# Optimization experiments

Hardware: AMD Instinct MI355X
Metric: run time of the kernel (lower is better)

## Reference

```python
import jax, jax.numpy as jnp
import numpy as np

N_CELLS = 2048
D_IN = 512
D_HID = 1024
D_OUT = 512
SYNC = 0.15
DEBATE = 0.15
N_FACTIONS = 8


def setup_inputs() -> dict:
    key = jax.random.key(0)
    ks = jax.random.split(key, 24)
    def w(k, shape, s=0.02):
        return jax.random.normal(k, shape, dtype=jnp.float32) * s
    ein = D_IN + D_HID          # complex-engine input dim (1536)
    gin = D_OUT + 1 + D_HID     # GRU gate input dim (1537)
    return {
        "x": jax.random.normal(ks[0], (1, D_IN), dtype=jnp.float32),
        "h_re": w(ks[1], (N_CELLS, D_HID), 0.1),
        "h_im": w(ks[2], (N_CELLS, D_HID), 0.1),
        "ea_wr": w(ks[3], (ein, D_OUT)), "ea_br": w(ks[4], (D_OUT,)),
        "ea_wi": w(ks[5], (ein, D_OUT)), "ea_bi": w(ks[6], (D_OUT,)),
        "eg_wr": w(ks[7], (ein, D_OUT)), "eg_br": w(ks[8], (D_OUT,)),
        "eg_wi": w(ks[9], (ein, D_OUT)), "eg_bi": w(ks[10], (D_OUT,)),
        "gz_w": w(ks[11], (gin, D_HID)), "gz_b": w(ks[12], (D_HID,)),
        "gr_w": w(ks[13], (gin, D_HID)), "gr_b": w(ks[14], (D_HID,)),
        "ghr_w": w(ks[15], (gin, D_HID)), "ghr_b": w(ks[16], (D_HID,)),
        "ghi_w": w(ks[17], (gin, D_HID)), "ghi_b": w(ks[18], (D_HID,)),
        "oh_w": w(ks[19], (2 * D_OUT, D_IN)), "oh_b": w(ks[20], (D_IN,)),
        "step": 7,
    }


def _clin(a, b, Wr, br, Wi, bi):
    # complex linear: (Wr + iWi)(a + ib) with torch's bias semantics
    return (a @ Wr + br) - (b @ Wi + bi), (b @ Wr + br) + (a @ Wi + bi)


def reference(x, h_re, h_im, ea_wr, ea_br, ea_wi, ea_bi, eg_wr, eg_br, eg_wi, eg_bi,
              gz_w, gz_b, gr_w, gr_b, ghr_w, ghr_b, ghi_w, ghi_b, oh_w, oh_b, step):
    # batch the 256-cell Python loop into single GEMMs over the cell axis
    xb = jnp.broadcast_to(x, (N_CELLS, D_IN))
    c_re = jnp.concatenate([xb, h_re], -1)                       # [N, D_IN+D_HID]
    c_im = jnp.concatenate([jnp.zeros_like(xb), h_im], -1)
    a_re, a_im = _clin(c_re, c_im, ea_wr, ea_br, ea_wi, ea_bi)
    g_re, g_im = _clin(c_re, c_im, eg_wr, eg_br, eg_wi, eg_bi)
    o_re, o_im = a_re - g_re, a_im - g_im                        # [N, D_OUT]
    tension = jnp.mean(o_re**2 + o_im**2, -1)                    # [N]

    # GRU memory update (detached input, matching output.detach())
    so_re = jax.lax.stop_gradient(o_re)
    so_im = jax.lax.stop_gradient(o_im)
    t_sg = jax.lax.stop_gradient(tension)
    mem_re = jnp.concatenate([so_re, t_sg[:, None]], -1)         # [N, D_OUT+1]
    mem_im = jnp.concatenate([so_im, jnp.zeros((N_CELLS, 1), o_im.dtype)], -1)
    x_mag = jnp.sqrt(mem_re**2 + mem_im**2)
    h_mag = jnp.sqrt(h_re**2 + h_im**2)
    cm = jnp.concatenate([x_mag, h_mag], -1)                     # [N, D_OUT+1+D_HID]
    z = jax.nn.sigmoid(cm @ gz_w + gz_b)
    r = jax.nn.sigmoid(cm @ gr_w + gr_b)
    comb_r = jnp.concatenate([mem_re, r * h_re], -1)
    comb_i = jnp.concatenate([mem_im, r * h_im], -1)
    cand_re = jnp.tanh(comb_r @ ghr_w + ghr_b)
    cand_im = jnp.tanh(comb_i @ ghi_w + ghi_b)
    nh_re = jax.lax.stop_gradient((1 - z) * h_re + z * cand_re)
    nh_im = jax.lax.stop_gradient((1 - z) * h_im + z * cand_im)

    # faction sync + debate (linear op, applied per component)
    fs = N_CELLS // N_FACTIONS
    def sync(h):
        hf = h.reshape(N_FACTIONS, fs, D_HID)
        hf = (1 - SYNC) * hf + SYNC * jnp.mean(hf, 1, keepdims=True)
        if step > 5:
            glob = jnp.mean(jnp.mean(hf, 1), 0)                  # [D_HID]
            dc = max(1, fs // 4)
            hf = hf.at[:, :dc].set((1 - DEBATE) * hf[:, :dc] + DEBATE * glob)
        return hf.reshape(N_CELLS, D_HID)
    nh_re, nh_im = sync(nh_re), sync(nh_im)

    # tension-softmax-weighted combination (weights are non-differentiable, .item() in torch)
    w_soft = jax.nn.softmax(t_sg)                                # [N]
    comb_re = (w_soft[:, None] * o_re).sum(0, keepdims=True)     # [1, D_OUT]
    comb_im = (w_soft[:, None] * o_im).sum(0, keepdims=True)
    out_real = jnp.concatenate([comb_re, comb_im], -1)           # [1, 2*D_OUT]
    pred = out_real @ oh_w + oh_b                                # [1, D_IN]
    return pred, jnp.mean(tension), nh_re, nh_im
```

## Files before the change

kernel.cpp:

```cpp
#include <hip/hip_runtime.h>
#include <math.h>

#define N_CELLS 2048
#define D_IN 512
#define D_HID 1024
#define D_OUT 512

typedef __attribute__((ext_vector_type(8))) short bf16x8;
typedef __attribute__((ext_vector_type(4))) float f32x4;
typedef __attribute__((ext_vector_type(4))) short short4v;

#define MFMA16(a, b, c) __builtin_amdgcn_mfma_f32_16x16x32_bf16(a, b, c, 0, 0, 0)

__device__ __forceinline__ short f2bf(float f) {
  union { float f; unsigned u; } v; v.f = f;
  unsigned r = (v.u + 0x7FFFu + ((v.u >> 16) & 1u)) >> 16;
  return (short)r;
}

__device__ __forceinline__ float bf2f(unsigned short u) {
  union { unsigned u; float f; } v; v.u = ((unsigned)u) << 16; return v.f;
}

__device__ __forceinline__ void gl_lds16(const void* g, void* l) {
  __builtin_amdgcn_global_load_lds(
      (const __attribute__((address_space(1))) void*)g,
      (__attribute__((address_space(3))) void*)l, 16, 0, 0);
}

__global__ __launch_bounds__(256) void k_prep_all(
    const float* __restrict__ w0, const float* __restrict__ w1,
    const float* __restrict__ w2, const float* __restrict__ w3,
    short* __restrict__ t0, short* __restrict__ t1,
    short* __restrict__ t2, short* __restrict__ t3,
    const float* __restrict__ ea_wr, const float* __restrict__ eg_wr,
    const float* __restrict__ ea_wi, const float* __restrict__ eg_wi,
    short* __restrict__ wdrT, short* __restrict__ wdiT, short* __restrict__ wdnT,
    const float* __restrict__ h_re, const float* __restrict__ h_im,
    short* __restrict__ hbre, short* __restrict__ hbim, short* __restrict__ gatesA,
    float* __restrict__ tens,
    const float* __restrict__ x,
    float* __restrict__ bpartr, float* __restrict__ bparti,
    float* __restrict__ fsbuf) {
  __shared__ float ts0[32][33], ts1[32][33];
  const int bx = blockIdx.x;
  const int tid = threadIdx.x;
  if (bx < 6144) {
    const int z = bx / 1536, idx = bx % 1536;
    const int xx = idx % 48, yy = idx / 48;
    const float* w = (z == 0) ? w0 : (z == 1) ? w1 : (z == 2) ? w2 : w3;
    short* wT = (z == 0) ? t0 : (z == 1) ? t1 : (z == 2) ? t2 : t3;
    const int k0 = xx * 32, n0 = yy * 32;
    const int c = tid & 31, r4 = tid >> 5;
#pragma unroll
    for (int i = 0; i < 4; ++i) {
      int kl = r4 * 4 + i;
      int k = k0 + kl;
      int srcrow = (k < 512) ? k : k + 1;
      ts0[kl][c] = w[(size_t)srcrow * D_HID + n0 + c];
    }
    __syncthreads();
#pragma unroll
    for (int i = 0; i < 4; ++i) {
      int nl = r4 * 4 + i;
      wT[(size_t)(n0 + nl) * 1536 + k0 + c] = f2bf(ts0[c][nl]);
    }
  } else if (bx < 6656) {
    const int idx = bx - 6144;
    const int xx = idx & 31, yy = idx >> 5;
    const int k0 = xx * 32, n0 = yy * 32;
    const int c = tid & 31, r4 = tid >> 5;
#pragma unroll
    for (int i = 0; i < 4; ++i) {
      int kl = r4 * 4 + i;
      int src = (512 + k0 + kl) * D_OUT + n0 + c;
      ts0[kl][c] = ea_wr[src] - eg_wr[src];
      ts1[kl][c] = ea_wi[src] - eg_wi[src];
    }
    __syncthreads();
#pragma unroll
    for (int i = 0; i < 4; ++i) {
      int nl = r4 * 4 + i;
      int dst = (n0 + nl) * D_HID + k0 + c;
      float dr = ts0[c][nl], di = ts1[c][nl];
      wdrT[dst] = f2bf(dr);
      wdiT[dst] = f2bf(di);
      wdnT[dst] = f2bf(-di);
    }
  } else if (bx < 8704) {
    const int idx = bx - 6656;
    if (tid == 0) tens[idx] = 0.f;
    int idx4 = (idx * 256 + tid) * 4;
    int m = idx4 >> 10, n = idx4 & 1023;
    float4 hr = *(const float4*)&h_re[idx4];
    float4 hi = *(const float4*)&h_im[idx4];
    short4v br, bi, bm;
    br.x = f2bf(hr.x); br.y = f2bf(hr.y); br.z = f2bf(hr.z); br.w = f2bf(hr.w);
    bi.x = f2bf(hi.x); bi.y = f2bf(hi.y); bi.z = f2bf(hi.z); bi.w = f2bf(hi.w);
    bm.x = f2bf(sqrtf(hr.x * hr.x + hi.x * hi.x));
    bm.y = f2bf(sqrtf(hr.y * hr.y + hi.y * hi.y));
    bm.z = f2bf(sqrtf(hr.z * hr.z + hi.z * hi.z));
    bm.w = f2bf(sqrtf(hr.w * hr.w + hi.w * hi.w));
    *(short4v*)&hbre[idx4] = br;
    *(short4v*)&hbim[idx4] = bi;
    *(short4v*)&gatesA[(size_t)m * 1536 + 512 + n] = bm;
  } else if (bx < 8720) {
    const int idx = bx - 8704;
    int n = (idx & 1) * 256 + tid;
    int kc = idx >> 1;
    float sr = 0.f, si = 0.f;
    for (int i = 0; i < 64; ++i) {
      int k = kc * 64 + i;
      float xv = x[k];
      int j = k * D_OUT + n;
      sr += xv * (ea_wr[j] - eg_wr[j]);
      si += xv * (ea_wi[j] - eg_wi[j]);
    }
    bpartr[kc * D_OUT + n] = sr;
    bparti[kc * D_OUT + n] = si;
  } else {
    const int idx = bx - 8720;
    int i = idx * 1024 + tid * 4;
    *(float4*)&fsbuf[i] = (float4){0.f, 0.f, 0.f, 0.f};
  }
}

__global__ __launch_bounds__(256) void k_engine(
    const short* __restrict__ hbre, const short* __restrict__ hbim,
    const short* __restrict__ wdrT, const short* __restrict__ wdiT,
    const short* __restrict__ wdnT,
    const float* __restrict__ bpartr, const float* __restrict__ bparti,
    const float* __restrict__ ea_br, const float* __restrict__ ea_bi,
    const float* __restrict__ eg_br, const float* __restrict__ eg_bi,
    float* __restrict__ ore, float* __restrict__ oim,
    short* __restrict__ gatesA, short* __restrict__ candAre, short* __restrict__ candAim,
    float* __restrict__ tens) {
  __shared__ short Ar[2 * 64 * 32], Ai[2 * 64 * 32];
  __shared__ short Brs[2 * 32 * 32], Bis[2 * 32 * 32], Bns[2 * 32 * 32];
  const int m0 = blockIdx.x * 64, n0 = blockIdx.y * 32;
  const int tid = threadIdx.x;
  const int wid = tid >> 6, lane = tid & 63;
  const int quad = lane >> 4, lcol = lane & 15;
  const int wm = wid * 16;
  f32x4 accre[2], accim[2];
#pragma unroll
  for (int nt = 0; nt < 2; ++nt) {
    accre[nt] = (f32x4){0.f, 0.f, 0.f, 0.f};
    accim[nt] = (f32x4){0.f, 0.f, 0.f, 0.f};
  }
  for (int k0 = 0; k0 < D_HID; k0 += 64) {
    if (k0) __syncthreads();
#pragma unroll
    for (int i = 0; i < 2; ++i) {
      int c = i * 256 + tid;
      int kh = c >> 8, row = (c >> 2) & 63, kq = c & 3;
      size_t g = (size_t)(m0 + row) * D_HID + k0 + kh * 32 + kq * 8;
      gl_lds16(hbre + g, &Ar[c * 8]);
      gl_lds16(hbim + g, &Ai[c * 8]);
    }
    {
      int c = tid;
      int kh = c >> 7, row = (c >> 2) & 31, kq = c & 3;
      size_t g = (size_t)(n0 + row) * D_HID + k0 + kh * 32 + kq * 8;
      gl_lds16(wdrT + g, &Brs[c * 8]);
      gl_lds16(wdiT + g, &Bis[c * 8]);
      gl_lds16(wdnT + g, &Bns[c * 8]);
    }
    __syncthreads();
#pragma unroll
    for (int kh = 0; kh < 2; ++kh) {
      bf16x8 ar, ai, br[2], bi[2], bn[2];
      int aoff = kh * 2048 + (wm + lcol) * 32 + quad * 8;
      ar = *(const bf16x8*)&Ar[aoff];
      ai = *(const bf16x8*)&Ai[aoff];
#pragma unroll
      for (int nt = 0; nt < 2; ++nt) {
        int boff = kh * 1024 + (nt * 16 + lcol) * 32 + quad * 8;
        br[nt] = *(const bf16x8*)&Brs[boff];
        bi[nt] = *(const bf16x8*)&Bis[boff];
        bn[nt] = *(const bf16x8*)&Bns[boff];
      }
#pragma unroll
      for (int nt = 0; nt < 2; ++nt) {
        accre[nt] = MFMA16(ar, br[nt], accre[nt]);
        accre[nt] = MFMA16(ai, bn[nt], accre[nt]);
        accim[nt] = MFMA16(ar, bi[nt], accim[nt]);
        accim[nt] = MFMA16(ai, br[nt], accim[nt]);
      }
    }
  }
  float biasre[2], biasim[2];
#pragma unroll
  for (int nt = 0; nt < 2; ++nt) {
    int n = n0 + nt * 16 + lcol;
    float sr = 0.f, si = 0.f;
#pragma unroll
    for (int kc = 0; kc < 8; ++kc) { sr += bpartr[kc * D_OUT + n]; si += bparti[kc * D_OUT + n]; }
    float brd = ea_br[n] - eg_br[n];
    float bid = ea_bi[n] - eg_bi[n];
    biasre[nt] = sr + brd - bid;
    biasim[nt] = si + brd + bid;
  }
#pragma unroll
  for (int r = 0; r < 4; ++r) {
    int m = m0 + wm + quad * 4 + r;
    float t = 0.f;
#pragma unroll
    for (int nt = 0; nt < 2; ++nt) {
      int n = n0 + nt * 16 + lcol;
      float cre = accre[nt][r] + biasre[nt];
      float cim = accim[nt][r] + biasim[nt];
      t += cre * cre + cim * cim;
      ore[(size_t)m * D_OUT + n] = cre;
      oim[(size_t)m * D_OUT + n] = cim;
      gatesA[(size_t)m * 1536 + n] = f2bf(sqrtf(cre * cre + cim * cim));
      candAre[(size_t)m * 1536 + n] = f2bf(cre);
      candAim[(size_t)m * 1536 + n] = f2bf(cim);
    }
#pragma unroll
    for (int off = 1; off < 16; off <<= 1) t += __shfl_xor(t, off);
    if (lcol == 0) atomicAdd(&tens[m], t * (1.f / 512.f));
  }
}

__global__ __launch_bounds__(256) void k_gates(
    const short* __restrict__ gatesA,
    const short* __restrict__ gzwT, const short* __restrict__ grwT,
    const float* __restrict__ gz_w, const float* __restrict__ gz_b,
    const float* __restrict__ gr_w, const float* __restrict__ gr_b,
    const float* __restrict__ tens,
    const float* __restrict__ h_re, const float* __restrict__ h_im,
    unsigned short* __restrict__ zbuf,
    short* __restrict__ candAre, short* __restrict__ candAim) {
  __shared__ short As[2 * 64 * 32];
  __shared__ short Bs[2 * 64 * 32];
  const int is_z = (blockIdx.z == 0);
  const short* Bt = is_z ? gzwT : grwT;
  const int m0 = blockIdx.x * 64, n0 = blockIdx.y * 64;
  const int tid = threadIdx.x;
  const int wid = tid >> 6, lane = tid & 63;
  const int quad = lane >> 4, lcol = lane & 15;
  const int wm = (wid >> 1) * 32, wn = (wid & 1) * 32;
  f32x4 acc[2][2];
#pragma unroll
  for (int mt = 0; mt < 2; ++mt)
#pragma unroll
    for (int nt = 0; nt < 2; ++nt) acc[mt][nt] = (f32x4){0.f, 0.f, 0.f, 0.f};
  for (int k0 = 0; k0 < 1536; k0 += 64) {
    if (k0) __syncthreads();
#pragma unroll
    for (int i = 0; i < 2; ++i) {
      int c = i * 256 + tid;
      int kh = c >> 8, row = (c >> 2) & 63, kq = c & 3;
      gl_lds16(gatesA + (size_t)(m0 + row) * 1536 + k0 + kh * 32 + kq * 8, &As[c * 8]);
      gl_lds16(Bt + (size_t)(n0 + row) * 1536 + k0 + kh * 32 + kq * 8, &Bs[c * 8]);
    }
    __syncthreads();
#pragma unroll
    for (int kh = 0; kh < 2; ++kh) {
      bf16x8 a[2], b[2];
#pragma unroll
      for (int mt = 0; mt < 2; ++mt)
        a[mt] = *(const bf16x8*)&As[kh * 2048 + (wm + mt * 16 + lcol) * 32 + quad * 8];
#pragma unroll
      for (int nt = 0; nt < 2; ++nt)
        b[nt] = *(const bf16x8*)&Bs[kh * 2048 + (wn + nt * 16 + lcol) * 32 + quad * 8];
#pragma unroll
      for (int mt = 0; mt < 2; ++mt)
#pragma unroll
        for (int nt = 0; nt < 2; ++nt)
          acc[mt][nt] = MFMA16(a[mt], b[nt], acc[mt][nt]);
    }
  }
#pragma unroll
  for (int mt = 0; mt < 2; ++mt)
#pragma unroll
    for (int nt = 0; nt < 2; ++nt)
#pragma unroll
      for (int r = 0; r < 4; ++r) {
        int m = m0 + wm + mt * 16 + quad * 4 + r;
        int n = n0 + wn + nt * 16 + lcol;
        float tv = tens[m];
        if (is_z) {
          float zp = acc[mt][nt][r] + gz_b[n] + tv * gz_w[(size_t)512 * D_HID + n];
          zbuf[(size_t)m * D_HID + n] = (unsigned short)f2bf(1.f / (1.f + expf(-zp)));
        } else {
          float rp = acc[mt][nt][r] + gr_b[n] + tv * gr_w[(size_t)512 * D_HID + n];
          float rr = 1.f / (1.f + expf(-rp));
          candAre[(size_t)m * 1536 + 512 + n] = f2bf(rr * h_re[(size_t)m * D_HID + n]);
          candAim[(size_t)m * 1536 + 512 + n] = f2bf(rr * h_im[(size_t)m * D_HID + n]);
        }
      }
}

__global__ __launch_bounds__(256) void k_cand(
    const short* __restrict__ candAre, const short* __restrict__ candAim,
    const short* __restrict__ ghrwT, const short* __restrict__ ghiwT,
    const float* __restrict__ ghr_b, const float* __restrict__ ghi_b,
    const float* __restrict__ ghr_w,
    const float* __restrict__ tens, const unsigned short* __restrict__ zbuf,
    const float* __restrict__ h_re, const float* __restrict__ h_im,
    float* __restrict__ nhre, float* __restrict__ nhim) {
  __shared__ short As[2 * 64 * 32];
  __shared__ short Bs[2 * 64 * 32];
  const int is_re = (blockIdx.z == 0);
  const short* A = is_re ? candAre : candAim;
  const short* Bt = is_re ? ghrwT : ghiwT;
  const float* bias = is_re ? ghr_b : ghi_b;
  const float* h = is_re ? h_re : h_im;
  float* outp = is_re ? nhre : nhim;
  const int m0 = blockIdx.x * 64, n0 = blockIdx.y * 64;
  const int tid = threadIdx.x;
  const int wid = tid >> 6, lane = tid & 63;
  const int quad = lane >> 4, lcol = lane & 15;
  const int wm = (wid >> 1) * 32, wn = (wid & 1) * 32;
  f32x4 acc[2][2];
#pragma unroll
  for (int mt = 0; mt < 2; ++mt)
#pragma unroll
    for (int nt = 0; nt < 2; ++nt) acc[mt][nt] = (f32x4){0.f, 0.f, 0.f, 0.f};
  for (int k0 = 0; k0 < 1536; k0 += 64) {
    if (k0) __syncthreads();
#pragma unroll
    for (int i = 0; i < 2; ++i) {
      int c = i * 256 + tid;
      int kh = c >> 8, row = (c >> 2) & 63, kq = c & 3;
      gl_lds16(A + (size_t)(m0 + row) * 1536 + k0 + kh * 32 + kq * 8, &As[c * 8]);
      gl_lds16(Bt + (size_t)(n0 + row) * 1536 + k0 + kh * 32 + kq * 8, &Bs[c * 8]);
    }
    __syncthreads();
#pragma unroll
    for (int kh = 0; kh < 2; ++kh) {
      bf16x8 a[2], b[2];
#pragma unroll
      for (int mt = 0; mt < 2; ++mt)
        a[mt] = *(const bf16x8*)&As[kh * 2048 + (wm + mt * 16 + lcol) * 32 + quad * 8];
#pragma unroll
      for (int nt = 0; nt < 2; ++nt)
        b[nt] = *(const bf16x8*)&Bs[kh * 2048 + (wn + nt * 16 + lcol) * 32 + quad * 8];
#pragma unroll
      for (int mt = 0; mt < 2; ++mt)
#pragma unroll
        for (int nt = 0; nt < 2; ++nt)
          acc[mt][nt] = MFMA16(a[mt], b[nt], acc[mt][nt]);
    }
  }
#pragma unroll
  for (int mt = 0; mt < 2; ++mt)
#pragma unroll
    for (int nt = 0; nt < 2; ++nt)
#pragma unroll
      for (int r = 0; r < 4; ++r) {
        int m = m0 + wm + mt * 16 + quad * 4 + r;
        int n = n0 + wn + nt * 16 + lcol;
        float pre = acc[mt][nt][r] + bias[n];
        if (is_re) pre += tens[m] * ghr_w[(size_t)512 * D_HID + n];
        float cand = tanhf(pre);
        float z = bf2f(zbuf[(size_t)m * D_HID + n]);
        float hv = h[(size_t)m * D_HID + n];
        outp[(size_t)m * D_HID + n] = (1.f - z) * hv + z * cand;
      }
}

__global__ __launch_bounds__(256) void k_fsum_part(
    const float* __restrict__ nhre, const float* __restrict__ nhim,
    float* __restrict__ fsbuf) {
  int f = blockIdx.x >> 3, rc = blockIdx.x & 7, comp = blockIdx.y;
  const float* src = comp ? nhim : nhre;
  float* fs = fsbuf + (size_t)comp * 8192;
  int row0 = f * 256 + rc * 32;
#pragma unroll
  for (int nc = 0; nc < 4; ++nc) {
    int n = nc * 256 + threadIdx.x;
    float s = 0.f;
    const float* base = src + (size_t)row0 * D_HID + n;
    for (int j = 0; j < 32; ++j) s += base[(size_t)j * D_HID];
    atomicAdd(&fs[(size_t)n * 8 + f], s);
  }
}

__global__ __launch_bounds__(256) void k_sync(
    float* __restrict__ nhre, float* __restrict__ nhim,
    const float* __restrict__ fsbuf, const int* __restrict__ step) {
  int idx = blockIdx.x * 256 + threadIdx.x;
  int m = idx >> 10, n = idx & 1023;
  int f = m >> 8;
  const float* f0 = fsbuf + (size_t)n * 8;
  const float* f1 = fsbuf + 8192 + (size_t)n * 8;
  float gr = 0.f, gi = 0.f;
#pragma unroll
  for (int ff = 0; ff < 8; ++ff) { gr += f0[ff]; gi += f1[ff]; }
  float fr = f0[f], fi = f1[f];
  float vr = nhre[idx], vi = nhim[idx];
  vr = 0.85f * vr + 0.15f * (fr * (1.f / 256.f));
  vi = 0.85f * vi + 0.15f * (fi * (1.f / 256.f));
  if (step[0] > 5 && (m & 255) < 64) {
    vr = 0.85f * vr + 0.15f * (gr * (1.f / 2048.f));
    vi = 0.85f * vi + 0.15f * (gi * (1.f / 2048.f));
  }
  nhre[idx] = vr;
  nhim[idx] = vi;
}

__global__ __launch_bounds__(1024) void k_stats(
    const float* __restrict__ tens, float* __restrict__ wsoft,
    float* __restrict__ meanT_out) {
  __shared__ float red[16];
  __shared__ float s_max, s_sum;
  int tid = threadIdx.x;
  int wid = tid >> 6, lane = tid & 63;
  float a = tens[tid], b = tens[tid + 1024];
  float mx = fmaxf(a, b);
  for (int off = 32; off; off >>= 1) mx = fmaxf(mx, __shfl_down(mx, off));
  if (lane == 0) red[wid] = mx;
  __syncthreads();
  if (tid == 0) {
    float m2 = red[0];
    for (int i = 1; i < 16; ++i) m2 = fmaxf(m2, red[i]);
    s_max = m2;
  }
  __syncthreads();
  float mxv = s_max;
  float ea = expf(a - mxv), eb = expf(b - mxv);
  float se = ea + eb;
  for (int off = 32; off; off >>= 1) se += __shfl_down(se, off);
  __syncthreads();
  if (lane == 0) red[wid] = se;
  __syncthreads();
  if (tid == 0) {
    float s2 = 0.f;
    for (int i = 0; i < 16; ++i) s2 += red[i];
    s_sum = s2;
  }
  __syncthreads();
  float inv = 1.f / s_sum;
  wsoft[tid] = ea * inv;
  wsoft[tid + 1024] = eb * inv;
  float st = a + b;
  for (int off = 32; off; off >>= 1) st += __shfl_down(st, off);
  __syncthreads();
  if (lane == 0) red[wid] = st;
  __syncthreads();
  if (tid == 0) {
    float s2 = 0.f;
    for (int i = 0; i < 16; ++i) s2 += red[i];
    meanT_out[0] = s2 * (1.f / 2048.f);
  }
}

__global__ __launch_bounds__(256) void k_comb_part(
    const float* __restrict__ ore, const float* __restrict__ oim,
    const float* __restrict__ wsoft, float* __restrict__ cpart) {
  int j = blockIdx.x * 256 + threadIdx.x;
  int mc = blockIdx.y;
  const float* src = (j < 512) ? ore : oim;
  int col = j & 511;
  float s = 0.f;
  for (int i = 0; i < 128; ++i) {
    int m = mc * 128 + i;
    s += wsoft[m] * src[(size_t)m * D_OUT + col];
  }
  cpart[(size_t)mc * 1024 + j] = s;
}

__global__ __launch_bounds__(256) void k_pred_part(
    const float* __restrict__ cpart, const float* __restrict__ oh_w,
    float* __restrict__ ppart) {
  __shared__ float combs[128];
  int tid = threadIdx.x;
  int jc = blockIdx.y;
  if (tid < 128) {
    float s = 0.f;
#pragma unroll
    for (int mc = 0; mc < 16; ++mc) s += cpart[(size_t)mc * 1024 + jc * 128 + tid];
    combs[tid] = s;
  }
  __syncthreads();
  int n = blockIdx.x * 256 + tid;
  float s = 0.f;
  for (int i = 0; i < 128; ++i)
    s += combs[i] * oh_w[(size_t)(jc * 128 + i) * D_IN + n];
  ppart[(size_t)jc * D_IN + n] = s;
}

__global__ __launch_bounds__(256) void k_pred_red(
    const float* __restrict__ ppart, const float* __restrict__ oh_b,
    float* __restrict__ pred) {
  int n = blockIdx.x * 256 + threadIdx.x;
  float s = oh_b[n];
#pragma unroll
  for (int jc = 0; jc < 8; ++jc) s += ppart[(size_t)jc * D_IN + n];
  pred[n] = s;
}

extern "C" void kernel_launch(void* const* d_in, const int* in_sizes, int n_in,
                              void* d_out, int out_size, void* d_ws, size_t ws_size,
                              hipStream_t stream) {
  const float* x     = (const float*)d_in[0];
  const float* h_re  = (const float*)d_in[1];
  const float* h_im  = (const float*)d_in[2];
  const float* ea_wr = (const float*)d_in[3];
  const float* ea_br = (const float*)d_in[4];
  const float* ea_wi = (const float*)d_in[5];
  const float* ea_bi = (const float*)d_in[6];
  const float* eg_wr = (const float*)d_in[7];
  const float* eg_br = (const float*)d_in[8];
  const float* eg_wi = (const float*)d_in[9];
  const float* eg_bi = (const float*)d_in[10];
  const float* gz_w  = (const float*)d_in[11];
  const float* gz_b  = (const float*)d_in[12];
  const float* gr_w  = (const float*)d_in[13];
  const float* gr_b  = (const float*)d_in[14];
  const float* ghr_w = (const float*)d_in[15];
  const float* ghr_b = (const float*)d_in[16];
  const float* ghi_w = (const float*)d_in[17];
  const float* ghi_b = (const float*)d_in[18];
  const float* oh_w  = (const float*)d_in[19];
  const float* oh_b  = (const float*)d_in[20];
  const int*   step  = (const int*)d_in[21];

  float* out = (float*)d_out;
  float* pred_out  = out;
  float* meanT_out = out + 512;
  float* nhre_out  = out + 513;
  float* nhim_out  = out + 513 + N_CELLS * D_HID;

  char* p = (char*)d_ws;
  auto carve = [&](size_t bytes) { char* r = p; p += (bytes + 255) & ~(size_t)255; return r; };
  short* wdrT   = (short*)carve(512 * 1024 * 2);
  short* wdiT   = (short*)carve(512 * 1024 * 2);
  short* wdnT   = (short*)carve(512 * 1024 * 2);
  short* gzwT   = (short*)carve(1024 * 1536 * 2);
  short* grwT   = (short*)carve(1024 * 1536 * 2);
  short* ghrwT  = (short*)carve(1024 * 1536 * 2);
  short* ghiwT  = (short*)carve(1024 * 1536 * 2);
  short* hbre   = (short*)carve(2048 * 1024 * 2);
  short* hbim   = (short*)carve(2048 * 1024 * 2);
  short* gatesA = (short*)carve((size_t)2048 * 1536 * 2);
  short* candAre= (short*)carve((size_t)2048 * 1536 * 2);
  short* candAim= (short*)carve((size_t)2048 * 1536 * 2);
  float* ore    = (float*)carve(2048 * 512 * 4);
  float* oim    = (float*)carve(2048 * 512 * 4);
  unsigned short* zbuf = (unsigned short*)carve((size_t)2048 * 1024 * 2);
  float* bpartr = (float*)carve(8 * 512 * 4);
  float* bparti = (float*)carve(8 * 512 * 4);
  float* tens   = (float*)carve(2048 * 4);
  float* fsbuf  = (float*)carve(2 * 8192 * 4);
  float* wsoft  = (float*)carve(2048 * 4);
  float* cpart  = (float*)carve(16 * 1024 * 4);
  float* ppart  = (float*)carve(8 * 512 * 4);

  hipLaunchKernelGGL(k_prep_all, dim3(8736), dim3(256), 0, stream,
                     gz_w, gr_w, ghr_w, ghi_w, gzwT, grwT, ghrwT, ghiwT,
                     ea_wr, eg_wr, ea_wi, eg_wi, wdrT, wdiT, wdnT,
                     h_re, h_im, hbre, hbim, gatesA, tens,
                     x, bpartr, bparti, fsbuf);
  hipLaunchKernelGGL(k_engine, dim3(32, 16), dim3(256), 0, stream,
                     hbre, hbim, wdrT, wdiT, wdnT,
                     bpartr, bparti, ea_br, ea_bi, eg_br, eg_bi,
                     ore, oim, gatesA, candAre, candAim, tens);
  hipLaunchKernelGGL(k_gates, dim3(32, 16, 2), dim3(256), 0, stream,
                     gatesA, gzwT, grwT, gz_w, gz_b, gr_w, gr_b, tens,
                     h_re, h_im, zbuf, candAre, candAim);
  hipLaunchKernelGGL(k_cand, dim3(32, 16, 2), dim3(256), 0, stream,
                     candAre, candAim, ghrwT, ghiwT, ghr_b, ghi_b, ghr_w,
                     tens, zbuf, h_re, h_im, nhre_out, nhim_out);
  hipLaunchKernelGGL(k_fsum_part, dim3(64, 2), dim3(256), 0, stream,
                     nhre_out, nhim_out, fsbuf);
  hipLaunchKernelGGL(k_sync, dim3((N_CELLS * D_HID) / 256), dim3(256), 0, stream,
                     nhre_out, nhim_out, fsbuf, step);
  hipLaunchKernelGGL(k_stats, dim3(1), dim3(1024), 0, stream, tens, wsoft, meanT_out);
  hipLaunchKernelGGL(k_comb_part, dim3(4, 16), dim3(256), 0, stream,
                     ore, oim, wsoft, cpart);
  hipLaunchKernelGGL(k_pred_part, dim3(2, 8), dim3(256), 0, stream, cpart, oh_w, ppart);
  hipLaunchKernelGGL(k_pred_red, dim3(2), dim3(256), 0, stream, ppart, oh_b, pred_out);
}
```

Before: 283.7 us.

## Fuse all stages into one cooperative persistent kernel with grid syncs

Replaces the ten separate launches with a single cooperative kernel of 512 blocks that loops over work units for each stage and separates stages with grid-wide syncs. The original per-stage kernels remain as a fallback. It also drops the precomputed negated-imaginary weight matrix in favour of sign-flipping the A fragment in registers, and merges sync with the comb step. The aim is to remove launch gaps and some memory traffic. In exchange, a 512-block grid on 256 CUs leaves each stage with fewer concurrent blocks than before, and grid syncs carry their own cost.

```diff
diff --git a/kernel.cpp b/kernel.cpp
--- a/kernel.cpp
+++ b/kernel.cpp
@@ -1,5 +1,8 @@
 #include <hip/hip_runtime.h>
+#include <hip/hip_cooperative_groups.h>
 #include <math.h>
+
+namespace cg = cooperative_groups;
 
 #define N_CELLS 2048
 #define D_IN 512
@@ -22,78 +25,89 @@
   union { unsigned u; float f; } v; v.u = ((unsigned)u) << 16; return v.f;
 }
 
+__device__ __forceinline__ bf16x8 neg8(bf16x8 v) {
+  union { bf16x8 s; unsigned u[4]; } a; a.s = v;
+#pragma unroll
+  for (int i = 0; i < 4; ++i) a.u[i] ^= 0x80008000u;
+  return a.s;
+}
+
 __device__ __forceinline__ void gl_lds16(const void* g, void* l) {
   __builtin_amdgcn_global_load_lds(
       (const __attribute__((address_space(1))) void*)g,
       (__attribute__((address_space(3))) void*)l, 16, 0, 0);
 }
 
-__global__ __launch_bounds__(256) void k_prep_all(
-    const float* __restrict__ w0, const float* __restrict__ w1,
-    const float* __restrict__ w2, const float* __restrict__ w3,
-    short* __restrict__ t0, short* __restrict__ t1,
-    short* __restrict__ t2, short* __restrict__ t3,
-    const float* __restrict__ ea_wr, const float* __restrict__ eg_wr,
-    const float* __restrict__ ea_wi, const float* __restrict__ eg_wi,
-    short* __restrict__ wdrT, short* __restrict__ wdiT, short* __restrict__ wdnT,
-    const float* __restrict__ h_re, const float* __restrict__ h_im,
-    short* __restrict__ hbre, short* __restrict__ hbim, short* __restrict__ gatesA,
-    float* __restrict__ tens,
-    const float* __restrict__ x,
-    float* __restrict__ bpartr, float* __restrict__ bparti,
-    float* __restrict__ fsbuf) {
-  __shared__ float ts0[32][33], ts1[32][33];
-  const int bx = blockIdx.x;
-  const int tid = threadIdx.x;
-  if (bx < 6144) {
-    const int z = bx / 1536, idx = bx % 1536;
+struct P {
+  const float *x, *h_re, *h_im;
+  const float *ea_wr, *ea_br, *ea_wi, *ea_bi;
+  const float *eg_wr, *eg_br, *eg_wi, *eg_bi;
+  const float *gz_w, *gz_b, *gr_w, *gr_b;
+  const float *ghr_w, *ghr_b, *ghi_w, *ghi_b;
+  const float *oh_w, *oh_b;
+  const int *step;
+  short *wdrT, *wdiT, *gzwT, *grwT, *ghrwT, *ghiwT;
+  short *hbre, *hbim, *gatesA, *candAre, *candAim;
+  float *ore, *oim;
+  unsigned short *zbuf;
+  float *bpartr, *bparti, *tens, *fsbuf, *wsoft, *cpart, *ppart;
+  float *pred_out, *meanT_out, *nhre, *nhim;
+};
+
+
+__device__ __forceinline__ void dev_prep(const P& p, int u, int tid, short* lds) {
+  if (u < 6144) {
+    float* ts0 = (float*)lds;
+    const int z = u / 1536, idx = u % 1536;
     const int xx = idx % 48, yy = idx / 48;
-    const float* w = (z == 0) ? w0 : (z == 1) ? w1 : (z == 2) ? w2 : w3;
-    short* wT = (z == 0) ? t0 : (z == 1) ? t1 : (z == 2) ? t2 : t3;
+    const float* w = (z == 0) ? p.gz_w : (z == 1) ? p.gr_w : (z == 2) ? p.ghr_w : p.ghi_w;
+    short* wT = (z == 0) ? p.gzwT : (z == 1) ? p.grwT : (z == 2) ? p.ghrwT : p.ghiwT;
     const int k0 = xx * 32, n0 = yy * 32;
     const int c = tid & 31, r4 = tid >> 5;
+    __syncthreads();
 #pragma unroll
     for (int i = 0; i < 4; ++i) {
       int kl = r4 * 4 + i;
       int k = k0 + kl;
       int srcrow = (k < 512) ? k : k + 1;
-      ts0[kl][c] = w[(size_t)srcrow * D_HID + n0 + c];
+      ts0[kl * 33 + c] = w[(size_t)srcrow * D_HID + n0 + c];
     }
     __syncthreads();
 #pragma unroll
     for (int i = 0; i < 4; ++i) {
       int nl = r4 * 4 + i;
-      wT[(size_t)(n0 + nl) * 1536 + k0 + c] = f2bf(ts0[c][nl]);
-    }
-  } else if (bx < 6656) {
-    const int idx = bx - 6144;
+      wT[(size_t)(n0 + nl) * 1536 + k0 + c] = f2bf(ts0[c * 33 + nl]);
+    }
+  } else if (u < 6656) {
+    float* ts0 = (float*)lds;
+    float* ts1 = ts0 + 32 * 33;
+    const int idx = u - 6144;
     const int xx = idx & 31, yy = idx >> 5;
     const int k0 = xx * 32, n0 = yy * 32;
     const int c = tid & 31, r4 = tid >> 5;
+    __syncthreads();
 #pragma unroll
     for (int i = 0; i < 4; ++i) {
       int kl = r4 * 4 + i;
       int src = (512 + k0 + kl) * D_OUT + n0 + c;
-      ts0[kl][c] = ea_wr[src] - eg_wr[src];
-      ts1[kl][c] = ea_wi[src] - eg_wi[src];
+      ts0[kl * 33 + c] = p.ea_wr[src] - p.eg_wr[src];
+      ts1[kl * 33 + c] = p.ea_wi[src] - p.eg_wi[src];
     }
     __syncthreads();
 #pragma unroll
     for (int i = 0; i < 4; ++i) {
       int nl = r4 * 4 + i;
       int dst = (n0 + nl) * D_HID + k0 + c;
-      float dr = ts0[c][nl], di = ts1[c][nl];
-      wdrT[dst] = f2bf(dr);
-      wdiT[dst] = f2bf(di);
-      wdnT[dst] = f2bf(-di);
-    }
-  } else if (bx < 8704) {
-    const int idx = bx - 6656;
-    if (tid == 0) tens[idx] = 0.f;
+      p.wdrT[dst] = f2bf(ts0[c * 33 + nl]);
+      p.wdiT[dst] = f2bf(ts1[c * 33 + nl]);
+    }
+  } else if (u < 8704) {
+    const int idx = u - 6656;
+    if (tid == 0) p.tens[idx] = 0.f;
     int idx4 = (idx * 256 + tid) * 4;
     int m = idx4 >> 10, n = idx4 & 1023;
-    float4 hr = *(const float4*)&h_re[idx4];
-    float4 hi = *(const float4*)&h_im[idx4];
+    float4 hr = *(const float4*)&p.h_re[idx4];
+    float4 hi = *(const float4*)&p.h_im[idx4];
     short4v br, bi, bm;
     br.x = f2bf(hr.x); br.y = f2bf(hr.y); br.z = f2bf(hr.z); br.w = f2bf(hr.w);
     bi.x = f2bf(hi.x); bi.y = f2bf(hi.y); bi.z = f2bf(hi.z); bi.w = f2bf(hi.w);
@@ -101,46 +115,38 @@
     bm.y = f2bf(sqrtf(hr.y * hr.y + hi.y * hi.y));
     bm.z = f2bf(sqrtf(hr.z * hr.z + hi.z * hi.z));
     bm.w = f2bf(sqrtf(hr.w * hr.w + hi.w * hi.w));
-    *(short4v*)&hbre[idx4] = br;
-    *(short4v*)&hbim[idx4] = bi;
-    *(short4v*)&gatesA[(size_t)m * 1536 + 512 + n] = bm;
-  } else if (bx < 8720) {
-    const int idx = bx - 8704;
+    *(short4v*)&p.hbre[idx4] = br;
+    *(short4v*)&p.hbim[idx4] = bi;
+    *(short4v*)&p.gatesA[(size_t)m * 1536 + 512 + n] = bm;
+  } else if (u < 8720) {
+    const int idx = u - 8704;
     int n = (idx & 1) * 256 + tid;
     int kc = idx >> 1;
     float sr = 0.f, si = 0.f;
     for (int i = 0; i < 64; ++i) {
       int k = kc * 64 + i;
-      float xv = x[k];
+      float xv = p.x[k];
       int j = k * D_OUT + n;
-      sr += xv * (ea_wr[j] - eg_wr[j]);
-      si += xv * (ea_wi[j] - eg_wi[j]);
-    }
-    bpartr[kc * D_OUT + n] = sr;
-    bparti[kc * D_OUT + n] = si;
+      sr += xv * (p.ea_wr[j] - p.eg_wr[j]);
+      si += xv * (p.ea_wi[j] - p.eg_wi[j]);
+    }
+    p.bpartr[kc * D_OUT + n] = sr;
+    p.bparti[kc * D_OUT + n] = si;
   } else {
-    const int idx = bx - 8720;
+    const int idx = u - 8720;
     int i = idx * 1024 + tid * 4;
-    *(float4*)&fsbuf[i] = (float4){0.f, 0.f, 0.f, 0.f};
-  }
-}
-
-__global__ __launch_bounds__(256) void k_engine(
-    const short* __restrict__ hbre, const short* __restrict__ hbim,
-    const short* __restrict__ wdrT, const short* __restrict__ wdiT,
-    const short* __restrict__ wdnT,
-    const float* __restrict__ bpartr, const float* __restrict__ bparti,
-    const float* __restrict__ ea_br, const float* __restrict__ ea_bi,
-    const float* __restrict__ eg_br, const float* __restrict__ eg_bi,
-    float* __restrict__ ore, float* __restrict__ oim,
-    short* __restrict__ gatesA, short* __restrict__ candAre, short* __restrict__ candAim,
-    float* __restrict__ tens) {
-  __shared__ short Ar[2 * 64 * 32], Ai[2 * 64 * 32];
-  __shared__ short Brs[2 * 32 * 32], Bis[2 * 32 * 32], Bns[2 * 32 * 32];
-  const int m0 = blockIdx.x * 64, n0 = blockIdx.y * 32;
-  const int tid = threadIdx.x;
+    *(float4*)&p.fsbuf[i] = (float4){0.f, 0.f, 0.f, 0.f};
+  }
+}
+
+__device__ __forceinline__ void dev_engine(const P& p, int unit, int tid, short* lds) {
+  short* Ar = lds;
+  short* Ai = lds + 4096;
+  short* Brs = lds + 8192;
+  short* Bis = lds + 10240;
   const int wid = tid >> 6, lane = tid & 63;
   const int quad = lane >> 4, lcol = lane & 15;
+  const int m0 = (unit & 31) * 64, n0 = (unit >> 5) * 32;
   const int wm = wid * 16;
   f32x4 accre[2], accim[2];
 #pragma unroll
@@ -149,27 +155,26 @@
     accim[nt] = (f32x4){0.f, 0.f, 0.f, 0.f};
   }
   for (int k0 = 0; k0 < D_HID; k0 += 64) {
-    if (k0) __syncthreads();
+    __syncthreads();
 #pragma unroll
     for (int i = 0; i < 2; ++i) {
       int c = i * 256 + tid;
       int kh = c >> 8, row = (c >> 2) & 63, kq = c & 3;
       size_t g = (size_t)(m0 + row) * D_HID + k0 + kh * 32 + kq * 8;
-      gl_lds16(hbre + g, &Ar[c * 8]);
-      gl_lds16(hbim + g, &Ai[c * 8]);
+      gl_lds16(p.hbre + g, &Ar[c * 8]);
+      gl_lds16(p.hbim + g, &Ai[c * 8]);
     }
     {
       int c = tid;
       int kh = c >> 7, row = (c >> 2) & 31, kq = c & 3;
       size_t g = (size_t)(n0 + row) * D_HID + k0 + kh * 32 + kq * 8;
-      gl_lds16(wdrT + g, &Brs[c * 8]);
-      gl_lds16(wdiT + g, &Bis[c * 8]);
-      gl_lds16(wdnT + g, &Bns[c * 8]);
+      gl_lds16(p.wdrT + g, &Brs[c * 8]);
+      gl_lds16(p.wdiT + g, &Bis[c * 8]);
     }
     __syncthreads();
 #pragma unroll
     for (int kh = 0; kh < 2; ++kh) {
-      bf16x8 ar, ai, br[2], bi[2], bn[2];
+      bf16x8 ar, ai, br[2], bi[2];
       int aoff = kh * 2048 + (wm + lcol) * 32 + quad * 8;
       ar = *(const bf16x8*)&Ar[aoff];
       ai = *(const bf16x8*)&Ai[aoff];
@@ -178,12 +183,12 @@
         int boff = kh * 1024 + (nt * 16 + lcol) * 32 + quad * 8;
         br[nt] = *(const bf16x8*)&Brs[boff];
         bi[nt] = *(const bf16x8*)&Bis[boff];
-        bn[nt] = *(const bf16x8*)&Bns[boff];
       }
+      bf16x8 ani = neg8(ai);
 #pragma unroll
       for (int nt = 0; nt < 2; ++nt) {
         accre[nt] = MFMA16(ar, br[nt], accre[nt]);
-        accre[nt] = MFMA16(ai, bn[nt], accre[nt]);
+        accre[nt] = MFMA16(ani, bi[nt], accre[nt]);
         accim[nt] = MFMA16(ar, bi[nt], accim[nt]);
         accim[nt] = MFMA16(ai, br[nt], accim[nt]);
       }
@@ -195,9 +200,9 @@
     int n = n0 + nt * 16 + lcol;
     float sr = 0.f, si = 0.f;
 #pragma unroll
-    for (int kc = 0; kc < 8; ++kc) { sr += bpartr[kc * D_OUT + n]; si += bparti[kc * D_OUT + n]; }
-    float brd = ea_br[n] - eg_br[n];
-    float bid = ea_bi[n] - eg_bi[n];
+    for (int kc = 0; kc < 8; ++kc) { sr += p.bpartr[kc * D_OUT + n]; si += p.bparti[kc * D_OUT + n]; }
+    float brd = p.ea_br[n] - p.eg_br[n];
+    float bid = p.ea_bi[n] - p.eg_bi[n];
     biasre[nt] = sr + brd - bid;
     biasim[nt] = si + brd + bid;
   }
@@ -211,35 +216,27 @@
       float cre = accre[nt][r] + biasre[nt];
       float cim = accim[nt][r] + biasim[nt];
       t += cre * cre + cim * cim;
-      ore[(size_t)m * D_OUT + n] = cre;
-      oim[(size_t)m * D_OUT + n] = cim;
-      gatesA[(size_t)m * 1536 + n] = f2bf(sqrtf(cre * cre + cim * cim));
-      candAre[(size_t)m * 1536 + n] = f2bf(cre);
-      candAim[(size_t)m * 1536 + n] = f2bf(cim);
+      p.ore[(size_t)m * D_OUT + n] = cre;
+      p.oim[(size_t)m * D_OUT + n] = cim;
+      p.gatesA[(size_t)m * 1536 + n] = f2bf(sqrtf(cre * cre + cim * cim));
+      p.candAre[(size_t)m * 1536 + n] = f2bf(cre);
+      p.candAim[(size_t)m * 1536 + n] = f2bf(cim);
     }
 #pragma unroll
     for (int off = 1; off < 16; off <<= 1) t += __shfl_xor(t, off);
-    if (lcol == 0) atomicAdd(&tens[m], t * (1.f / 512.f));
-  }
-}
-
-__global__ __launch_bounds__(256) void k_gates(
-    const short* __restrict__ gatesA,
-    const short* __restrict__ gzwT, const short* __restrict__ grwT,
-    const float* __restrict__ gz_w, const float* __restrict__ gz_b,
-    const float* __restrict__ gr_w, const float* __restrict__ gr_b,
-    const float* __restrict__ tens,
-    const float* __restrict__ h_re, const float* __restrict__ h_im,
-    unsigned short* __restrict__ zbuf,
-    short* __restrict__ candAre, short* __restrict__ candAim) {
-  __shared__ short As[2 * 64 * 32];
-  __shared__ short Bs[2 * 64 * 32];
-  const int is_z = (blockIdx.z == 0);
-  const short* Bt = is_z ? gzwT : grwT;
-  const int m0 = blockIdx.x * 64, n0 = blockIdx.y * 64;
-  const int tid = threadIdx.x;
+    if (lcol == 0) atomicAdd(&p.tens[m], t * (1.f / 512.f));
+  }
+}
+
+__device__ __forceinline__ void dev_gates(const P& p, int unit, int tid, short* lds) {
+  short* As = lds;
+  short* Bs = lds + 4096;
+  const int is_z = (unit < 512);
+  const int bb = unit & 511;
+  const short* Bt = is_z ? p.gzwT : p.grwT;
   const int wid = tid >> 6, lane = tid & 63;
   const int quad = lane >> 4, lcol = lane & 15;
+  const int m0 = (bb & 31) * 64, n0 = (bb >> 5) * 64;
   const int wm = (wid >> 1) * 32, wn = (wid & 1) * 32;
   f32x4 acc[2][2];
 #pragma unroll
@@ -247,12 +244,12 @@
 #pragma unroll
     for (int nt = 0; nt < 2; ++nt) acc[mt][nt] = (f32x4){0.f, 0.f, 0.f, 0.f};
   for (int k0 = 0; k0 < 1536; k0 += 64) {
-    if (k0) __syncthreads();
+    __syncthreads();
 #pragma unroll
     for (int i = 0; i < 2; ++i) {
       int c = i * 256 + tid;
       int kh = c >> 8, row = (c >> 2) & 63, kq = c & 3;
-      gl_lds16(gatesA + (size_t)(m0 + row) * 1536 + k0 + kh * 32 + kq * 8, &As[c * 8]);
+      gl_lds16(p.gatesA + (size_t)(m0 + row) * 1536 + k0 + kh * 32 + kq * 8, &As[c * 8]);
       gl_lds16(Bt + (size_t)(n0 + row) * 1536 + k0 + kh * 32 + kq * 8, &Bs[c * 8]);
     }
     __syncthreads();
@@ -280,39 +277,32 @@
       for (int r = 0; r < 4; ++r) {
         int m = m0 + wm + mt * 16 + quad * 4 + r;
         int n = n0 + wn + nt * 16 + lcol;
-        float tv = tens[m];
+        float tv = p.tens[m];
         if (is_z) {
-          float zp = acc[mt][nt][r] + gz_b[n] + tv * gz_w[(size_t)512 * D_HID + n];
-          zbuf[(size_t)m * D_HID + n] = (unsigned short)f2bf(1.f / (1.f + expf(-zp)));
+          float zp = acc[mt][nt][r] + p.gz_b[n] + tv * p.gz_w[(size_t)512 * D_HID + n];
+          p.zbuf[(size_t)m * D_HID + n] = (unsigned short)f2bf(1.f / (1.f + expf(-zp)));
         } else {
-          float rp = acc[mt][nt][r] + gr_b[n] + tv * gr_w[(size_t)512 * D_HID + n];
+          float rp = acc[mt][nt][r] + p.gr_b[n] + tv * p.gr_w[(size_t)512 * D_HID + n];
           float rr = 1.f / (1.f + expf(-rp));
-          candAre[(size_t)m * 1536 + 512 + n] = f2bf(rr * h_re[(size_t)m * D_HID + n]);
-          candAim[(size_t)m * 1536 + 512 + n] = f2bf(rr * h_im[(size_t)m * D_HID + n]);
+          p.candAre[(size_t)m * 1536 + 512 + n] = f2bf(rr * p.h_re[(size_t)m * D_HID + n]);
+          p.candAim[(size_t)m * 1536 + 512 + n] = f2bf(rr * p.h_im[(size_t)m * D_HID + n]);
         }
       }
 }
 
-__global__ __launch_bounds__(256) void k_cand(
-    const short* __restrict__ candAre, const short* __restrict__ candAim,
-    const short* __restrict__ ghrwT, const short* __restrict__ ghiwT,
-    const float* __restrict__ ghr_b, const float* __restrict__ ghi_b,
-    const float* __restrict__ ghr_w,
-    const float* __restrict__ tens, const unsigned short* __restrict__ zbuf,
-    const float* __restrict__ h_re, const float* __restrict__ h_im,
-    float* __restrict__ nhre, float* __restrict__ nhim) {
-  __shared__ short As[2 * 64 * 32];
-  __shared__ short Bs[2 * 64 * 32];
-  const int is_re = (blockIdx.z == 0);
-  const short* A = is_re ? candAre : candAim;
-  const short* Bt = is_re ? ghrwT : ghiwT;
-  const float* bias = is_re ? ghr_b : ghi_b;
-  const float* h = is_re ? h_re : h_im;
-  float* outp = is_re ? nhre : nhim;
-  const int m0 = blockIdx.x * 64, n0 = blockIdx.y * 64;
-  const int tid = threadIdx.x;
+__device__ __forceinline__ void dev_cand(const P& p, int unit, int tid, short* lds) {
+  short* As = lds;
+  short* Bs = lds + 4096;
+  const int is_re = (unit < 512);
+  const int bb = unit & 511;
+  const short* A = is_re ? p.candAre : p.candAim;
+  const short* Bt = is_re ? p.ghrwT : p.ghiwT;
+  const float* bias = is_re ? p.ghr_b : p.ghi_b;
+  const float* h = is_re ? p.h_re : p.h_im;
+  float* outp = is_re ? p.nhre : p.nhim;
   const int wid = tid >> 6, lane = tid & 63;
   const int quad = lane >> 4, lcol = lane & 15;
+  const int m0 = (bb & 31) * 64, n0 = (bb >> 5) * 64;
   const int wm = (wid >> 1) * 32, wn = (wid & 1) * 32;
   f32x4 acc[2][2];
 #pragma unroll
@@ -320,7 +310,7 @@
 #pragma unroll
     for (int nt = 0; nt < 2; ++nt) acc[mt][nt] = (f32x4){0.f, 0.f, 0.f, 0.f};
   for (int k0 = 0; k0 < 1536; k0 += 64) {
-    if (k0) __syncthreads();
+    __syncthreads();
 #pragma unroll
     for (int i = 0; i < 2; ++i) {
       int c = i * 256 + tid;
@@ -354,24 +344,22 @@
         int m = m0 + wm + mt * 16 + quad * 4 + r;
         int n = n0 + wn + nt * 16 + lcol;
         float pre = acc[mt][nt][r] + bias[n];
-        if (is_re) pre += tens[m] * ghr_w[(size_t)512 * D_HID + n];
+        if (is_re) pre += p.tens[m] * p.ghr_w[(size_t)512 * D_HID + n];
         float cand = tanhf(pre);
-        float z = bf2f(zbuf[(size_t)m * D_HID + n]);
+        float z = bf2f(p.zbuf[(size_t)m * D_HID + n]);
         float hv = h[(size_t)m * D_HID + n];
         outp[(size_t)m * D_HID + n] = (1.f - z) * hv + z * cand;
       }
 }
 
-__global__ __launch_bounds__(256) void k_fsum_part(
-    const float* __restrict__ nhre, const float* __restrict__ nhim,
-    float* __restrict__ fsbuf) {
-  int f = blockIdx.x >> 3, rc = blockIdx.x & 7, comp = blockIdx.y;
-  const float* src = comp ? nhim : nhre;
-  float* fs = fsbuf + (size_t)comp * 8192;
+__device__ __forceinline__ void dev_fsum(const P& p, int unit, int tid) {
+  int f = (unit & 63) >> 3, rc = unit & 7, comp = unit >> 6;
+  const float* src = comp ? p.nhim : p.nhre;
+  float* fs = p.fsbuf + (size_t)comp * 8192;
   int row0 = f * 256 + rc * 32;
 #pragma unroll
   for (int nc = 0; nc < 4; ++nc) {
-    int n = nc * 256 + threadIdx.x;
+    int n = nc * 256 + tid;
     float s = 0.f;
     const float* base = src + (size_t)row0 * D_HID + n;
     for (int j = 0; j < 32; ++j) s += base[(size_t)j * D_HID];
@@ -379,157 +367,159 @@
   }
 }
 
-__global__ __launch_bounds__(256) void k_sync(
-    float* __restrict__ nhre, float* __restrict__ nhim,
-    const float* __restrict__ fsbuf, const int* __restrict__ step) {
-  int idx = blockIdx.x * 256 + threadIdx.x;
-  int m = idx >> 10, n = idx & 1023;
-  int f = m >> 8;
-  const float* f0 = fsbuf + (size_t)n * 8;
-  const float* f1 = fsbuf + 8192 + (size_t)n * 8;
-  float gr = 0.f, gi = 0.f;
-#pragma unroll
-  for (int ff = 0; ff < 8; ++ff) { gr += f0[ff]; gi += f1[ff]; }
-  float fr = f0[f], fi = f1[f];
-  float vr = nhre[idx], vi = nhim[idx];
-  vr = 0.85f * vr + 0.15f * (fr * (1.f / 256.f));
-  vi = 0.85f * vi + 0.15f * (fi * (1.f / 256.f));
-  if (step[0] > 5 && (m & 255) < 64) {
-    vr = 0.85f * vr + 0.15f * (gr * (1.f / 2048.f));
-    vi = 0.85f * vi + 0.15f * (gi * (1.f / 2048.f));
-  }
-  nhre[idx] = vr;
-  nhim[idx] = vi;
-}
-
-__global__ __launch_bounds__(1024) void k_stats(
-    const float* __restrict__ tens, float* __restrict__ wsoft,
-    float* __restrict__ meanT_out) {
-  __shared__ float red[16];
-  __shared__ float s_max, s_sum;
-  int tid = threadIdx.x;
-  int wid = tid >> 6, lane = tid & 63;
-  float a = tens[tid], b = tens[tid + 1024];
-  float mx = fmaxf(a, b);
-  for (int off = 32; off; off >>= 1) mx = fmaxf(mx, __shfl_down(mx, off));
+__device__ __forceinline__ void dev_stats(const P& p, int tid, short* lds) {
+  float* red = (float*)lds;
+  const int wid = tid >> 6, lane = tid & 63;
+  float v[8];
+  float mx = -1e30f;
+#pragma unroll
+  for (int k2 = 0; k2 < 8; ++k2) { v[k2] = p.tens[tid + 256 * k2]; mx = fmaxf(mx, v[k2]); }
+  for (int off = 1; off < 64; off <<= 1) mx = fmaxf(mx, __shfl_xor(mx, off));
   if (lane == 0) red[wid] = mx;
   __syncthreads();
-  if (tid == 0) {
-    float m2 = red[0];
-    for (int i = 1; i < 16; ++i) m2 = fmaxf(m2, red[i]);
-    s_max = m2;
-  }
+  float gmax = fmaxf(fmaxf(red[0], red[1]), fmaxf(red[2], red[3]));
   __syncthreads();
-  float mxv = s_max;
-  float ea = expf(a - mxv), eb = expf(b - mxv);
-  float se = ea + eb;
-  for (int off = 32; off; off >>= 1) se += __shfl_down(se, off);
+  float e[8], ps = 0.f, pt = 0.f;
+#pragma unroll
+  for (int k2 = 0; k2 < 8; ++k2) { e[k2] = expf(v[k2] - gmax); ps += e[k2]; pt += v[k2]; }
+  for (int off = 1; off < 64; off <<= 1) ps += __shfl_xor(ps, off);
+  if (lane == 0) red[wid] = ps;
   __syncthreads();
-  if (lane == 0) red[wid] = se;
+  float gsum = red[0] + red[1] + red[2] + red[3];
   __syncthreads();
-  if (tid == 0) {
-    float s2 = 0.f;
-    for (int i = 0; i < 16; ++i) s2 += red[i];
-    s_sum = s2;
-  }
+  for (int off = 1; off < 64; off <<= 1) pt += __shfl_xor(pt, off);
+  if (lane == 0) red[wid] = pt;
   __syncthreads();
-  float inv = 1.f / s_sum;
-  wsoft[tid] = ea * inv;
-  wsoft[tid + 1024] = eb * inv;
-  float st = a + b;
-  for (int off = 32; off; off >>= 1) st += __shfl_down(st, off);
-  __syncthreads();
-  if (lane == 0) red[wid] = st;
-  __syncthreads();
-  if (tid == 0) {
-    float s2 = 0.f;
-    for (int i = 0; i < 16; ++i) s2 += red[i];
-    meanT_out[0] = s2 * (1.f / 2048.f);
-  }
-}
-
-__global__ __launch_bounds__(256) void k_comb_part(
-    const float* __restrict__ ore, const float* __restrict__ oim,
-    const float* __restrict__ wsoft, float* __restrict__ cpart) {
-  int j = blockIdx.x * 256 + threadIdx.x;
-  int mc = blockIdx.y;
-  const float* src = (j < 512) ? ore : oim;
-  int col = j & 511;
-  float s = 0.f;
-  for (int i = 0; i < 128; ++i) {
-    int m = mc * 128 + i;
-    s += wsoft[m] * src[(size_t)m * D_OUT + col];
-  }
-  cpart[(size_t)mc * 1024 + j] = s;
-}
-
-__global__ __launch_bounds__(256) void k_pred_part(
-    const float* __restrict__ cpart, const float* __restrict__ oh_w,
-    float* __restrict__ ppart) {
-  __shared__ float combs[128];
-  int tid = threadIdx.x;
-  int jc = blockIdx.y;
+  if (tid == 0) p.meanT_out[0] = (red[0] + red[1] + red[2] + red[3]) * (1.f / 2048.f);
+  float inv = 1.f / gsum;
+#pragma unroll
+  for (int k2 = 0; k2 < 8; ++k2) p.wsoft[tid + 256 * k2] = e[k2] * inv;
+}
+
+__device__ __forceinline__ void dev_syncomb(const P& p, int u, int tid) {
+  if (u < 8192) {
+    int idx = u * 256 + tid;
+    int m = idx >> 10, n = idx & 1023;
+    int f = m >> 8;
+    const float* f0 = p.fsbuf + (size_t)n * 8;
+    const float* f1 = p.fsbuf + 8192 + (size_t)n * 8;
+    float gr = 0.f, gi = 0.f;
+#pragma unroll
+    for (int ff = 0; ff < 8; ++ff) { gr += f0[ff]; gi += f1[ff]; }
+    float fr = f0[f], fi = f1[f];
+    float vr = p.nhre[idx], vi = p.nhim[idx];
+    vr = 0.85f * vr + 0.15f * (fr * (1.f / 256.f));
+    vi = 0.85f * vi + 0.15f * (fi * (1.f / 256.f));
+    if (p.step[0] > 5 && (m & 255) < 64) {
+      vr = 0.85f * vr + 0.15f * (gr * (1.f / 2048.f));
+      vi = 0.85f * vi + 0.15f * (gi * (1.f / 2048.f));
+    }
+    p.nhre[idx] = vr;
+    p.nhim[idx] = vi;
+  } else {
+    int v2 = u - 8192;
+    int j = (v2 & 3) * 256 + tid;
+    int mc = v2 >> 2;
+    const float* src = (j < 512) ? p.ore : p.oim;
+    int col = j & 511;
+    float s = 0.f;
+    for (int i = 0; i < 128; ++i) {
+      int m = mc * 128 + i;
+      s += p.wsoft[m] * src[(size_t)m * D_OUT + col];
+    }
+    p.cpart[(size_t)mc * 1024 + j] = s;
+  }
+}
+
+__device__ __forceinline__ void dev_predpart(const P& p, int unit, int tid, short* lds) {
+  float* combs = (float*)lds;
+  int jc = unit >> 1;
   if (tid < 128) {
     float s = 0.f;
 #pragma unroll
-    for (int mc = 0; mc < 16; ++mc) s += cpart[(size_t)mc * 1024 + jc * 128 + tid];
+    for (int mc = 0; mc < 16; ++mc) s += p.cpart[(size_t)mc * 1024 + jc * 128 + tid];
     combs[tid] = s;
   }
   __syncthreads();
-  int n = blockIdx.x * 256 + tid;
+  int n = (unit & 1) * 256 + tid;
   float s = 0.f;
   for (int i = 0; i < 128; ++i)
-    s += combs[i] * oh_w[(size_t)(jc * 128 + i) * D_IN + n];
-  ppart[(size_t)jc * D_IN + n] = s;
-}
-
-__global__ __launch_bounds__(256) void k_pred_red(
-    const float* __restrict__ ppart, const float* __restrict__ oh_b,
-    float* __restrict__ pred) {
-  int n = blockIdx.x * 256 + threadIdx.x;
-  float s = oh_b[n];
-#pragma unroll
-  for (int jc = 0; jc < 8; ++jc) s += ppart[(size_t)jc * D_IN + n];
-  pred[n] = s;
+    s += combs[i] * p.oh_w[(size_t)(jc * 128 + i) * D_IN + n];
+  p.ppart[(size_t)jc * D_IN + n] = s;
+}
+
+__device__ __forceinline__ void dev_predred(const P& p, int unit, int tid) {
+  int n = unit * 256 + tid;
+  float s = p.oh_b[n];
+#pragma unroll
+  for (int jc = 0; jc < 8; ++jc) s += p.ppart[(size_t)jc * D_IN + n];
+  p.pred_out[n] = s;
+}
+
+__global__ __launch_bounds__(256, 2) void k_mega(P p) {
+  __shared__ __align__(16) short lds[12288];
+  cg::grid_group grid = cg::this_grid();
+  const int bx = blockIdx.x;
+  const int tid = threadIdx.x;
+  for (int u = bx; u < 8736; u += 512) dev_prep(p, u, tid, lds);
+  grid.sync();
+  dev_engine(p, bx, tid, lds);
+  grid.sync();
+  for (int u = bx; u < 1024; u += 512) dev_gates(p, u, tid, lds);
+  grid.sync();
+  for (int u = bx; u < 1024; u += 512) dev_cand(p, u, tid, lds);
+  grid.sync();
+  if (bx < 128) dev_fsum(p, bx, tid);
+  else if (bx == 128) dev_stats(p, tid, lds);
+  grid.sync();
+  for (int u = bx; u < 8256; u += 512) dev_syncomb(p, u, tid);
+  grid.sync();
+  if (bx < 16) dev_predpart(p, bx, tid, lds);
+  grid.sync();
+  if (bx < 2) dev_predred(p, bx, tid);
+}
+
+__global__ __launch_bounds__(256) void k_prep_k(P p) {
+  __shared__ __align__(16) short lds[12288];
+  dev_prep(p, blockIdx.x, threadIdx.x, lds);
+}
+__global__ __launch_bounds__(256) void k_engine_k(P p) {
+  __shared__ __align__(16) short lds[12288];
+  dev_engine(p, blockIdx.x, threadIdx.x, lds);
+}
+__global__ __launch_bounds__(256) void k_gates_k(P p) {
+  __shared__ __align__(16) short lds[12288];
+  dev_gates(p, blockIdx.x, threadIdx.x, lds);
+}
+__global__ __launch_bounds__(256) void k_cand_k(P p) {
+  __shared__ __align__(16) short lds[12288];
+  dev_cand(p, blockIdx.x, threadIdx.x, lds);
+}
+__global__ __launch_bounds__(256) void k_fs_k(P p) {
+  __shared__ __align__(16) short lds[64];
+  if (blockIdx.x < 128) dev_fsum(p, blockIdx.x, threadIdx.x);
+  else dev_stats(p, threadIdx.x, lds);
+}
+__global__ __launch_bounds__(256) void k_sc_k(P p) {
+  dev_syncomb(p, blockIdx.x, threadIdx.x);
+}
+__global__ __launch_bounds__(256) void k_pp_k(P p) {
+  __shared__ __align__(16) short lds[256];
+  dev_predpart(p, blockIdx.x, threadIdx.x, lds);
+}
+__global__ __launch_bounds__(256) void k_pr_k(P p) {
+  dev_predred(p, blockIdx.x, threadIdx.x);
 }
 
 extern "C" void kernel_launch(void* const* d_in, const int* in_sizes, int n_in,
                               void* d_out, int out_size, void* d_ws, size_t ws_size,
                               hipStream_t stream) {
-  const float* x     = (const float*)d_in[0];
-  const float* h_re  = (const float*)d_in[1];
-  const float* h_im  = (const float*)d_in[2];
-  const float* ea_wr = (const float*)d_in[3];
-  const float* ea_br = (const float*)d_in[4];
-  const float* ea_wi = (const float*)d_in[5];
-  const float* ea_bi = (const float*)d_in[6];
-  const float* eg_wr = (const float*)d_in[7];
-  const float* eg_br = (const float*)d_in[8];
-  const float* eg_wi = (const float*)d_in[9];
-  const float* eg_bi = (const float*)d_in[10];
-  const float* gz_w  = (const float*)d_in[11];
-  const float* gz_b  = (const float*)d_in[12];
-  const float* gr_w  = (const float*)d_in[13];
-  const float* gr_b  = (const float*)d_in[14];
-  const float* ghr_w = (const float*)d_in[15];
-  const float* ghr_b = (const float*)d_in[16];
-  const float* ghi_w = (const float*)d_in[17];
-  const float* ghi_b = (const float*)d_in[18];
-  const float* oh_w  = (const float*)d_in[19];
-  const float* oh_b  = (const float*)d_in[20];
-  const int*   step  = (const int*)d_in[21];
-
   float* out = (float*)d_out;
-  float* pred_out  = out;
-  float* meanT_out = out + 512;
-  float* nhre_out  = out + 513;
-  float* nhim_out  = out + 513 + N_CELLS * D_HID;
-
-  char* p = (char*)d_ws;
-  auto carve = [&](size_t bytes) { char* r = p; p += (bytes + 255) & ~(size_t)255; return r; };
+
+  char* wp = (char*)d_ws;
+  auto carve = [&](size_t bytes) { char* r = wp; wp += (bytes + 255) & ~(size_t)255; return r; };
   short* wdrT   = (short*)carve(512 * 1024 * 2);
   short* wdiT   = (short*)carve(512 * 1024 * 2);
-  short* wdnT   = (short*)carve(512 * 1024 * 2);
   short* gzwT   = (short*)carve(1024 * 1536 * 2);
   short* grwT   = (short*)carve(1024 * 1536 * 2);
   short* ghrwT  = (short*)carve(1024 * 1536 * 2);
@@ -550,28 +540,65 @@
   float* cpart  = (float*)carve(16 * 1024 * 4);
   float* ppart  = (float*)carve(8 * 512 * 4);
 
-  hipLaunchKernelGGL(k_prep_all, dim3(8736), dim3(256), 0, stream,
-                     gz_w, gr_w, ghr_w, ghi_w, gzwT, grwT, ghrwT, ghiwT,
-                     ea_wr, eg_wr, ea_wi, eg_wi, wdrT, wdiT, wdnT,
-                     h_re, h_im, hbre, hbim, gatesA, tens,
-                     x, bpartr, bparti, fsbuf);
-  hipLaunchKernelGGL(k_engine, dim3(32, 16), dim3(256), 0, stream,
-                     hbre, hbim, wdrT, wdiT, wdnT,
-                     bpartr, bparti, ea_br, ea_bi, eg_br, eg_bi,
-                     ore, oim, gatesA, candAre, candAim, tens);
-  hipLaunchKernelGGL(k_gates, dim3(32, 16, 2), dim3(256), 0, stream,
-                     gatesA, gzwT, grwT, gz_w, gz_b, gr_w, gr_b, tens,
-                     h_re, h_im, zbuf, candAre, candAim);
-  hipLaunchKernelGGL(k_cand, dim3(32, 16, 2), dim3(256), 0, stream,
-                     candAre, candAim, ghrwT, ghiwT, ghr_b, ghi_b, ghr_w,
-                     tens, zbuf, h_re, h_im, nhre_out, nhim_out);
-  hipLaunchKernelGGL(k_fsum_part, dim3(64, 2), dim3(256), 0, stream,
-                     nhre_out, nhim_out, fsbuf);
-  hipLaunchKernelGGL(k_sync, dim3((N_CELLS * D_HID) / 256), dim3(256), 0, stream,
-                     nhre_out, nhim_out, fsbuf, step);
-  hipLaunchKernelGGL(k_stats, dim3(1), dim3(1024), 0, stream, tens, wsoft, meanT_out);
-  hipLaunchKernelGGL(k_comb_part, dim3(4, 16), dim3(256), 0, stream,
-                     ore, oim, wsoft, cpart);
-  hipLaunchKernelGGL(k_pred_part, dim3(2, 8), dim3(256), 0, stream, cpart, oh_w, ppart);
-  hipLaunchKernelGGL(k_pred_red, dim3(2), dim3(256), 0, stream, ppart, oh_b, pred_out);
-}
+  P prm;
+  prm.x     = (const float*)d_in[0];
+  prm.h_re  = (const float*)d_in[1];
+  prm.h_im  = (const float*)d_in[2];
+  prm.ea_wr = (const float*)d_in[3];
+  prm.ea_br = (const float*)d_in[4];
+  prm.ea_wi = (const float*)d_in[5];
+  prm.ea_bi = (const float*)d_in[6];
+  prm.eg_wr = (const float*)d_in[7];
+  prm.eg_br = (const float*)d_in[8];
+  prm.eg_wi = (const float*)d_in[9];
+  prm.eg_bi = (const float*)d_in[10];
+  prm.gz_w  = (const float*)d_in[11];
+  prm.gz_b  = (const float*)d_in[12];
+  prm.gr_w  = (const float*)d_in[13];
+  prm.gr_b  = (const float*)d_in[14];
+  prm.ghr_w = (const float*)d_in[15];
+  prm.ghr_b = (const float*)d_in[16];
+  prm.ghi_w = (const float*)d_in[17];
+  prm.ghi_b = (const float*)d_in[18];
+  prm.oh_w  = (const float*)d_in[19];
+  prm.oh_b  = (const float*)d_in[20];
+  prm.step  = (const int*)d_in[21];
+  prm.wdrT = wdrT; prm.wdiT = wdiT;
+  prm.gzwT = gzwT; prm.grwT = grwT; prm.ghrwT = ghrwT; prm.ghiwT = ghiwT;
+  prm.hbre = hbre; prm.hbim = hbim;
+  prm.gatesA = gatesA; prm.candAre = candAre; prm.candAim = candAim;
+  prm.ore = ore; prm.oim = oim; prm.zbuf = zbuf;
+  prm.bpartr = bpartr; prm.bparti = bparti;
+  prm.tens = tens; prm.fsbuf = fsbuf; prm.wsoft = wsoft;
+  prm.cpart = cpart; prm.ppart = ppart;
+  prm.pred_out = out;
+  prm.meanT_out = out + 512;
+  prm.nhre = out + 513;
+  prm.nhim = out + 513 + N_CELLS * D_HID;
+
+  int dev = 0;
+  (void)hipGetDevice(&dev);
+  int cus = 0;
+  (void)hipDeviceGetAttribute(&cus, hipDeviceAttributeMultiprocessorCount, dev);
+  int maxBlocksPerCU = 0;
+  hipError_t occErr = hipOccupancyMaxActiveBlocksPerMultiprocessor(&maxBlocksPerCU, k_mega, 256, 0);
+  bool coop_ok = (occErr == hipSuccess) && (cus > 0) &&
+                 ((long long)maxBlocksPerCU * cus >= 512);
+
+  hipError_t lerr = hipErrorUnknown;
+  if (coop_ok) {
+    void* args[] = { &prm };
+    lerr = hipLaunchCooperativeKernel((void*)k_mega, dim3(512), dim3(256), args, 0, stream);
+  }
+  if (lerr != hipSuccess) {
+    (void)hipGetLastError();
+    hipLaunchKernelGGL(k_prep_k, dim3(8736), dim3(256), 0, stream, prm);
+    hipLaunchKernelGGL(k_engine_k, dim3(512), dim3(256), 0, stream, prm);
+    hipLaunchKernelGGL(k_gates_k, dim3(1024), dim3(256), 0, stream, prm);
+    hipLaunchKernelGGL(k_cand_k, dim3(1024), dim3(256), 0, stream, prm);
+    hipLaunchKernelGGL(k_fs_k, dim3(129), dim3(256), 0, stream, prm);
+    hipLaunchKernelGGL(k_sc_k, dim3(8256), dim3(256), 0, stream, prm);
+    hipLaunchKernelGGL(k_pp_k, dim3(16), dim3(256), 0, stream, prm);
+    hipLaunchKernelGGL(k_pr_k, dim3(2), dim3(256), 0, stream, prm);
+  }
+}
```

Measured after the change: 725.8 us. 156% more time.
